# Optimization experiments

Measured on AMD Instinct MI355X. Metric: run time of the kernel, lower is better.

Reference implementation:

```python
import jax, jax.numpy as jnp
import numpy as np

NEG_INF = -1e9


def setup_inputs() -> dict:
    key = jax.random.key(0)
    k1, k2, k3, k4, k5, k6 = jax.random.split(key, 6)
    B, P, N, C, H = 32, 512, 64, 9, 128
    polylines = jax.random.normal(k1, (B, P, N, C), dtype=jnp.float32)
    polylines_mask = jax.random.uniform(k2, (B, P, N)) > 0.1
    # MLP params (Linear(C,H) -> ReLU -> Linear(H,H)), torch-style init scale
    W1 = jax.random.uniform(k3, (C, H), minval=-1.0, maxval=1.0) / jnp.sqrt(C)
    b1 = jax.random.uniform(k4, (H,), minval=-1.0, maxval=1.0) / jnp.sqrt(C)
    W2 = jax.random.uniform(k5, (H, H), minval=-1.0, maxval=1.0) / jnp.sqrt(H)
    b2 = jax.random.uniform(k6, (H,), minval=-1.0, maxval=1.0) / jnp.sqrt(H)
    return {"polylines": polylines, "polylines_mask": polylines_mask,
            "W1": W1, "b1": b1, "W2": W2, "b2": b2}


def reference(polylines, polylines_mask, W1, b1, W2, b2):
    # Point MLP applied to all points (invalid ones are overwritten below,
    # identical math to the torch masked-gather version).
    h = jax.nn.relu(jnp.einsum('bpnc,ch->bpnh', polylines, W1) + b1)
    feat = jnp.einsum('bpnh,hd->bpnd', h, W2) + b2  # [B,P,N,H]
    feat = jnp.where(polylines_mask[..., None], feat, NEG_INF)
    pooled = jnp.max(feat, axis=2)  # [B,P,H]
    # Polylines with no valid points pooled to NEG_INF -> zero them out.
    any_valid = jnp.any(polylines_mask, axis=2)  # [B,P]
    return jnp.where(any_valid[..., None], pooled, 0.0)
```

## Files before the change

### kernel.cpp

```cpp
#include <hip/hip_runtime.h>


using bf16x8 = __attribute__((ext_vector_type(8))) short;
using f32x4  = __attribute__((ext_vector_type(4))) float;

#define MFMA_BF16(A,B,C) __builtin_amdgcn_mfma_f32_16x16x32_bf16((A),(B),(C),0,0,0)

__device__ __forceinline__ unsigned short f2bf(float f) {
  union { float f; unsigned int u; } v; v.f = f;
  unsigned int r = v.u + 0x7fffu + ((v.u >> 16) & 1u);
  return (unsigned short)(r >> 16);
}

__device__ __forceinline__ unsigned int pack_bf2(float a, float b) {
  union { float f; unsigned int u; } ua, ub; ua.f = a; ub.f = b;
  return __builtin_amdgcn_perm(ub.u + 0x8000u, ua.u + 0x8000u, 0x07060302u);
}

__global__ void prep_kernel(const float* __restrict__ W1, const float* __restrict__ W2,
                            const void* __restrict__ mask,
                            unsigned short* __restrict__ w1t, unsigned short* __restrict__ w2t,
                            int* __restrict__ flag) {
  int b = blockIdx.x, t = threadIdx.x;
  if (b < 68) {
    int idx = b * 256 + t;
    if (idx < 128 * 136) {
      int d = idx / 136, h = idx - d * 136;
      float v = (h < 128) ? W2[h * 128 + d] : 0.f;
      w2t[idx] = f2bf(v);
    }
  } else if (b < 88) {
    int idx = (b - 68) * 256 + t;
    if (idx < 128 * 40) {
      int h = idx / 40, c = idx - h * 40;
      float v = (c < 9) ? W1[c * 128 + h] : 0.f;
      w1t[idx] = f2bf(v);
    }
  } else {
    __shared__ int cnt;
    if (t == 0) cnt = 0;
    __syncthreads();
    const unsigned char* mb = (const unsigned char*)mask;
    int local = 0;
    for (int i = t * 16; i < t * 16 + 16; i++) local += (mb[i] != 0) ? 1 : 0;
    atomicAdd(&cnt, local);
    __syncthreads();
    if (t == 0) *flag = (cnt > 2800) ? 1 : 0;
  }
}

__global__ __launch_bounds__(256, 4) void poly_main_k(
    const float* __restrict__ X, const void* __restrict__ mask,
    const float* __restrict__ b1g, const float* __restrict__ b2g,
    const unsigned short* __restrict__ w1t, const unsigned short* __restrict__ w2t,
    const int* __restrict__ flagp, float* __restrict__ out)
{
  __shared__ __align__(16) unsigned short Hb[128 * 136];

  const int tid  = threadIdx.x;
  const int lane = tid & 63;
  const int w    = tid >> 6;
  const int wr   = w >> 1, wc = w & 1;
  const int li   = lane & 15, q = lane >> 4;

  float mf[4];
  {
    int flag = *flagp;
    long long mbase = (long long)blockIdx.x * 128 + wc * 64 + li;
    if (flag) {
      const unsigned char* mp = (const unsigned char*)mask;
      #pragma unroll
      for (int tm = 0; tm < 4; tm++) mf[tm] = mp[mbase + tm * 16] ? 0.f : -4e9f;
    } else {
      const int* mp = (const int*)mask;
      #pragma unroll
      for (int tm = 0; tm < 4; tm++) mf[tm] = mp[mbase + tm * 16] ? 0.f : -4e9f;
    }
  }

  bf16x8 bx[4];
  {
    const float* xb = X + (long long)blockIdx.x * (128 * 9);
    #pragma unroll
    for (int tm = 0; tm < 4; tm++) {
      int m = wc * 64 + tm * 16 + li;
      const float* xr = xb + m * 9;
      union { bf16x8 v; unsigned int u[4]; } uu;
      uu.u[0] = uu.u[1] = uu.u[2] = uu.u[3] = 0u;
      if (q == 0) {
        uu.u[0] = pack_bf2(xr[0], xr[1]);
        uu.u[1] = pack_bf2(xr[2], xr[3]);
        uu.u[2] = pack_bf2(xr[4], xr[5]);
        uu.u[3] = pack_bf2(xr[6], xr[7]);
      } else if (q == 1) {
        uu.u[0] = pack_bf2(xr[8], 0.f);
      }
      bx[tm] = uu.v;
    }
  }

  f32x4 acc1[4][4];
  #pragma unroll
  for (int a = 0; a < 4; a++)
    #pragma unroll
    for (int b = 0; b < 4; b++) acc1[a][b] = f32x4{0.f, 0.f, 0.f, 0.f};
  {
    bf16x8 af[4];
    #pragma unroll
    for (int th = 0; th < 4; th++)
      af[th] = *(const bf16x8*)(w1t + (wr * 64 + th * 16 + li) * 40 + q * 8);
    #pragma unroll
    for (int th = 0; th < 4; th++)
      #pragma unroll
      for (int tm = 0; tm < 4; tm++)
        acc1[th][tm] = MFMA_BF16(af[th], bx[tm], acc1[th][tm]);
  }

  #pragma unroll
  for (int th = 0; th < 4; th++) {
    f32x4 bv = *(const f32x4*)(b1g + wr * 64 + th * 16 + q * 4);
    #pragma unroll
    for (int tm = 0; tm < 4; tm++) {
      int m = wc * 64 + tm * 16 + li;
      float v0 = fmaxf(acc1[th][tm][0] + bv[0], 0.f);
      float v1 = fmaxf(acc1[th][tm][1] + bv[1], 0.f);
      float v2 = fmaxf(acc1[th][tm][2] + bv[2], 0.f);
      float v3 = fmaxf(acc1[th][tm][3] + bv[3], 0.f);
      uint2 hv;
      hv.x = pack_bf2(v0, v1);
      hv.y = pack_bf2(v2, v3);
      *(uint2*)(Hb + m * 136 + wr * 64 + th * 16 + q * 4) = hv;
    }
  }
  __syncthreads();

  f32x4 acc2[4][4];
  #pragma unroll
  for (int a = 0; a < 4; a++)
    #pragma unroll
    for (int b = 0; b < 4; b++) acc2[a][b] = f32x4{0.f, 0.f, 0.f, 0.f};
  #pragma unroll
  for (int ks = 0; ks < 4; ks++) {
    bf16x8 af[4], bf[4];
    #pragma unroll
    for (int td = 0; td < 4; td++)
      af[td] = *(const bf16x8*)(w2t + (wr * 64 + td * 16 + li) * 136 + ks * 32 + q * 8);
    #pragma unroll
    for (int tm = 0; tm < 4; tm++)
      bf[tm] = *(const bf16x8*)(Hb + (wc * 64 + tm * 16 + li) * 136 + ks * 32 + q * 8);
    #pragma unroll
    for (int td = 0; td < 4; td++)
      #pragma unroll
      for (int tm = 0; tm < 4; tm++)
        acc2[td][tm] = MFMA_BF16(af[td], bf[tm], acc2[td][tm]);
  }

  f32x4 pooled[4];
  #pragma unroll
  for (int td = 0; td < 4; td++) {
    f32x4 bv = *(const f32x4*)(b2g + wr * 64 + td * 16 + q * 4);
    #pragma unroll
    for (int r = 0; r < 4; r++) {
      float v0 = acc2[td][0][r] + mf[0];
      float v1 = acc2[td][1][r] + mf[1];
      float v2 = acc2[td][2][r] + mf[2];
      float v3 = acc2[td][3][r] + mf[3];
      pooled[td][r] = fmaxf(fmaxf(v0, v1), fmaxf(v2, v3)) + bv[r];
    }
  }

  #pragma unroll
  for (int s = 8; s >= 1; s >>= 1) {
    #pragma unroll
    for (int td = 0; td < 4; td++) {
      #pragma unroll
      for (int r = 0; r < 4; r++) {
        float o = __shfl_xor(pooled[td][r], s, 64);
        pooled[td][r] = fmaxf(pooled[td][r], o);
      }
    }
  }

  if (li == 0) {
    long long poly = (long long)blockIdx.x * 2 + wc;
    #pragma unroll
    for (int td = 0; td < 4; td++) {
      f32x4 v = pooled[td];
      #pragma unroll
      for (int r = 0; r < 4; r++) if (v[r] < -1e8f) v[r] = 0.f;
      *(f32x4*)(out + poly * 128 + wr * 64 + td * 16 + q * 4) = v;
    }
  }
}

extern "C" void kernel_launch(void* const* d_in, const int* in_sizes, int n_in,
                              void* d_out, int out_size, void* d_ws, size_t ws_size,
                              hipStream_t stream) {
  const float* X    = (const float*)d_in[0];
  const void*  mask = d_in[1];
  const float* W1   = (const float*)d_in[2];
  const float* b1   = (const float*)d_in[3];
  const float* W2   = (const float*)d_in[4];
  const float* b2   = (const float*)d_in[5];
  float* out = (float*)d_out;

  unsigned short* w1t = (unsigned short*)d_ws;
  unsigned short* w2t = w1t + 128 * 40;
  int* flag = (int*)((char*)d_ws + 45056);

  prep_kernel<<<89, 256, 0, stream>>>(W1, W2, mask, w1t, w2t, flag);
  poly_main_k<<<8192, 256, 0, stream>>>(X, mask, b1, b2, w1t, w2t, flag, out);
}
```

Before: 168.1 us.

## Pre-swizzle weights to MFMA fragment order, stage X in LDS, bitpack mask

Weights are now pre-swizzled into per-lane MFMA fragment order, so each lane's global load is contiguous. The X tile is staged through shared memory with coalesced vector loads instead of strided 9-float row reads. A new prep kernel packs the mask into 64-bit ballot bitmasks so the main kernel reads one word per wave. The final pooling reduction moves from cross-lane shuffles to an LDS transpose with coalesced output stores, at the cost of an extra kernel launch and two additional barriers.

```diff
diff --git a/kernel.cpp b/kernel.cpp
--- a/kernel.cpp
+++ b/kernel.cpp
@@ -4,7 +4,7 @@
 using bf16x8 = __attribute__((ext_vector_type(8))) short;
 using f32x4  = __attribute__((ext_vector_type(4))) float;
 
-#define MFMA_BF16(A,B,C) __builtin_amdgcn_mfma_f32_16x16x32_bf16((A),(B),(C),0,0,0)
+#define MFMA32(A,B,C) __builtin_amdgcn_mfma_f32_16x16x32_bf16((A),(B),(C),0,0,0)
 
 __device__ __forceinline__ unsigned short f2bf(float f) {
   union { float f; unsigned int u; } v; v.f = f;
@@ -17,26 +17,12 @@
   return __builtin_amdgcn_perm(ub.u + 0x8000u, ua.u + 0x8000u, 0x07060302u);
 }
 
-__global__ void prep_kernel(const float* __restrict__ W1, const float* __restrict__ W2,
-                            const void* __restrict__ mask,
-                            unsigned short* __restrict__ w1t, unsigned short* __restrict__ w2t,
-                            int* __restrict__ flag) {
+__global__ void prep1(const float* __restrict__ W1, const float* __restrict__ W2,
+                      const void* __restrict__ mask,
+                      unsigned short* __restrict__ w1sw, unsigned short* __restrict__ w2sw,
+                      int* __restrict__ flag) {
   int b = blockIdx.x, t = threadIdx.x;
-  if (b < 68) {
-    int idx = b * 256 + t;
-    if (idx < 128 * 136) {
-      int d = idx / 136, h = idx - d * 136;
-      float v = (h < 128) ? W2[h * 128 + d] : 0.f;
-      w2t[idx] = f2bf(v);
-    }
-  } else if (b < 88) {
-    int idx = (b - 68) * 256 + t;
-    if (idx < 128 * 40) {
-      int h = idx / 40, c = idx - h * 40;
-      float v = (c < 9) ? W1[c * 128 + h] : 0.f;
-      w1t[idx] = f2bf(v);
-    }
-  } else {
+  if (b == 0) {
     __shared__ int cnt;
     if (t == 0) cnt = 0;
     __syncthreads();
@@ -46,15 +32,53 @@
     atomicAdd(&cnt, local);
     __syncthreads();
     if (t == 0) *flag = (cnt > 2800) ? 1 : 0;
-  }
+  } else if (b <= 2) {
+    int e = (b - 1) * 256 + t;
+    int lane = e & 63, grp = e >> 6;
+    int li = lane & 15, q = lane >> 4;
+    int h = grp * 16 + li;
+    int c0 = q * 8;
+    #pragma unroll
+    for (int j = 0; j < 8; j++) {
+      int c = c0 + j;
+      w1sw[e * 8 + j] = f2bf((c < 9) ? W1[c * 128 + h] : 0.f);
+    }
+  } else {
+    int e = (b - 3) * 256 + t;
+    if (e < 2048) {
+      int lane = e & 63, grp = e >> 6;
+      int wr = grp >> 4, sub = grp & 15;
+      int ks = sub >> 2, td = sub & 3;
+      int li = lane & 15, q = lane >> 4;
+      int d = wr * 64 + td * 16 + li;
+      int h0 = ks * 32 + q * 8;
+      #pragma unroll
+      for (int j = 0; j < 8; j++)
+        w2sw[e * 8 + j] = f2bf(W2[(h0 + j) * 128 + d]);
+    }
+  }
+}
+
+__global__ void prep2(const void* __restrict__ mask, const int* __restrict__ flagp,
+                      unsigned long long* __restrict__ bits) {
+  int gid = blockIdx.x * 256 + threadIdx.x;
+  int flag = *flagp;
+  bool v;
+  if (flag) v = ((const unsigned char*)mask)[gid] != 0;
+  else      v = ((const int*)mask)[gid] != 0;
+  unsigned long long bm = __ballot(v);
+  if ((threadIdx.x & 63) == 0)
+    bits[blockIdx.x * 4 + (threadIdx.x >> 6)] = bm;
 }
 
 __global__ __launch_bounds__(256, 4) void poly_main_k(
     const float* __restrict__ X, const void* __restrict__ mask,
     const float* __restrict__ b1g, const float* __restrict__ b2g,
-    const unsigned short* __restrict__ w1t, const unsigned short* __restrict__ w2t,
-    const int* __restrict__ flagp, float* __restrict__ out)
+    const unsigned short* __restrict__ w1sw, const unsigned short* __restrict__ w2sw,
+    const int* __restrict__ flagp, const unsigned long long* __restrict__ bits,
+    int use_bits, float* __restrict__ out)
 {
+  __shared__ __align__(16) float Xs[1152];
   __shared__ __align__(16) unsigned short Hb[128 * 136];
 
   const int tid  = threadIdx.x;
@@ -64,39 +88,47 @@
   const int li   = lane & 15, q = lane >> 4;
 
   float mf[4];
-  {
+  if (use_bits) {
+    unsigned long long bm = bits[(long long)blockIdx.x * 2 + wc];
+    #pragma unroll
+    for (int tm = 0; tm < 4; tm++)
+      mf[tm] = ((bm >> (tm * 16 + li)) & 1ull) ? 0.f : -4e9f;
+  } else {
     int flag = *flagp;
-    long long mbase = (long long)blockIdx.x * 128 + wc * 64 + li;
+    long long mb = (long long)blockIdx.x * 128 + wc * 64 + li;
     if (flag) {
       const unsigned char* mp = (const unsigned char*)mask;
       #pragma unroll
-      for (int tm = 0; tm < 4; tm++) mf[tm] = mp[mbase + tm * 16] ? 0.f : -4e9f;
+      for (int tm = 0; tm < 4; tm++) mf[tm] = mp[mb + tm * 16] ? 0.f : -4e9f;
     } else {
       const int* mp = (const int*)mask;
       #pragma unroll
-      for (int tm = 0; tm < 4; tm++) mf[tm] = mp[mbase + tm * 16] ? 0.f : -4e9f;
-    }
-  }
+      for (int tm = 0; tm < 4; tm++) mf[tm] = mp[mb + tm * 16] ? 0.f : -4e9f;
+    }
+  }
+
+  {
+    const f32x4* xg = (const f32x4*)(X + (long long)blockIdx.x * 1152);
+    f32x4* xl = (f32x4*)Xs;
+    xl[tid] = xg[tid];
+    if (tid < 32) xl[tid + 256] = xg[tid + 256];
+  }
+  __syncthreads();
 
   bf16x8 bx[4];
-  {
-    const float* xb = X + (long long)blockIdx.x * (128 * 9);
-    #pragma unroll
-    for (int tm = 0; tm < 4; tm++) {
-      int m = wc * 64 + tm * 16 + li;
-      const float* xr = xb + m * 9;
-      union { bf16x8 v; unsigned int u[4]; } uu;
-      uu.u[0] = uu.u[1] = uu.u[2] = uu.u[3] = 0u;
-      if (q == 0) {
-        uu.u[0] = pack_bf2(xr[0], xr[1]);
-        uu.u[1] = pack_bf2(xr[2], xr[3]);
-        uu.u[2] = pack_bf2(xr[4], xr[5]);
-        uu.u[3] = pack_bf2(xr[6], xr[7]);
-      } else if (q == 1) {
-        uu.u[0] = pack_bf2(xr[8], 0.f);
-      }
-      bx[tm] = uu.v;
-    }
+  #pragma unroll
+  for (int tm = 0; tm < 4; tm++) {
+    int m = wc * 64 + tm * 16 + li;
+    const float* xr = Xs + m * 9;
+    union { bf16x8 v; unsigned int u[4]; } uu;
+    uu.u[0] = uu.u[1] = uu.u[2] = uu.u[3] = 0u;
+    if (q == 0) {
+      uu.u[0] = pack_bf2(xr[0], xr[1]); uu.u[1] = pack_bf2(xr[2], xr[3]);
+      uu.u[2] = pack_bf2(xr[4], xr[5]); uu.u[3] = pack_bf2(xr[6], xr[7]);
+    } else if (q == 1) {
+      uu.u[0] = pack_bf2(xr[8], 0.f);
+    }
+    bx[tm] = uu.v;
   }
 
   f32x4 acc1[4][4];
@@ -105,15 +137,15 @@
     #pragma unroll
     for (int b = 0; b < 4; b++) acc1[a][b] = f32x4{0.f, 0.f, 0.f, 0.f};
   {
-    bf16x8 af[4];
+    bf16x8 a1[4];
     #pragma unroll
     for (int th = 0; th < 4; th++)
-      af[th] = *(const bf16x8*)(w1t + (wr * 64 + th * 16 + li) * 40 + q * 8);
+      a1[th] = *(const bf16x8*)(w1sw + ((wr * 4 + th) * 64 + lane) * 8);
     #pragma unroll
     for (int th = 0; th < 4; th++)
       #pragma unroll
       for (int tm = 0; tm < 4; tm++)
-        acc1[th][tm] = MFMA_BF16(af[th], bx[tm], acc1[th][tm]);
+        acc1[th][tm] = MFMA32(a1[th], bx[tm], acc1[th][tm]);
   }
 
   #pragma unroll
@@ -141,18 +173,18 @@
     for (int b = 0; b < 4; b++) acc2[a][b] = f32x4{0.f, 0.f, 0.f, 0.f};
   #pragma unroll
   for (int ks = 0; ks < 4; ks++) {
-    bf16x8 af[4], bf[4];
+    bf16x8 a2[4], bb[4];
     #pragma unroll
     for (int td = 0; td < 4; td++)
-      af[td] = *(const bf16x8*)(w2t + (wr * 64 + td * 16 + li) * 136 + ks * 32 + q * 8);
+      a2[td] = *(const bf16x8*)(w2sw + (((wr * 16 + ks * 4 + td) * 64) + lane) * 8);
     #pragma unroll
     for (int tm = 0; tm < 4; tm++)
-      bf[tm] = *(const bf16x8*)(Hb + (wc * 64 + tm * 16 + li) * 136 + ks * 32 + q * 8);
+      bb[tm] = *(const bf16x8*)(Hb + (wc * 64 + tm * 16 + li) * 136 + ks * 32 + q * 8);
     #pragma unroll
     for (int td = 0; td < 4; td++)
       #pragma unroll
       for (int tm = 0; tm < 4; tm++)
-        acc2[td][tm] = MFMA_BF16(af[td], bf[tm], acc2[td][tm]);
+        acc2[td][tm] = MFMA32(a2[td], bb[tm], acc2[td][tm]);
   }
 
   f32x4 pooled[4];
@@ -169,27 +201,21 @@
     }
   }
 
-  #pragma unroll
-  for (int s = 8; s >= 1; s >>= 1) {
-    #pragma unroll
-    for (int td = 0; td < 4; td++) {
-      #pragma unroll
-      for (int r = 0; r < 4; r++) {
-        float o = __shfl_xor(pooled[td][r], s, 64);
-        pooled[td][r] = fmaxf(pooled[td][r], o);
-      }
-    }
-  }
-
-  if (li == 0) {
-    long long poly = (long long)blockIdx.x * 2 + wc;
-    #pragma unroll
-    for (int td = 0; td < 4; td++) {
-      f32x4 v = pooled[td];
-      #pragma unroll
-      for (int r = 0; r < 4; r++) if (v[r] < -1e8f) v[r] = 0.f;
-      *(f32x4*)(out + poly * 128 + wr * 64 + td * 16 + q * 4) = v;
-    }
+  __syncthreads();
+  float* P = (float*)Hb;
+  #pragma unroll
+  for (int td = 0; td < 4; td++)
+    *(f32x4*)(P + (wc * 16 + li) * 132 + wr * 64 + td * 16 + q * 4) = pooled[td];
+  __syncthreads();
+
+  {
+    int p = tid >> 7, d = tid & 127;
+    const float* Pp = P + p * (16 * 132) + d;
+    float v = Pp[0];
+    #pragma unroll
+    for (int j = 1; j < 16; j++) v = fmaxf(v, Pp[j * 132]);
+    if (v < -1e8f) v = 0.f;
+    out[(long long)blockIdx.x * 256 + tid] = v;
   }
 }
 
@@ -204,10 +230,14 @@
   const float* b2   = (const float*)d_in[5];
   float* out = (float*)d_out;
 
-  unsigned short* w1t = (unsigned short*)d_ws;
-  unsigned short* w2t = w1t + 128 * 40;
-  int* flag = (int*)((char*)d_ws + 45056);
-
-  prep_kernel<<<89, 256, 0, stream>>>(W1, W2, mask, w1t, w2t, flag);
-  poly_main_k<<<8192, 256, 0, stream>>>(X, mask, b1, b2, w1t, w2t, flag, out);
-}
+  unsigned short* w1sw = (unsigned short*)d_ws;
+  unsigned short* w2sw = (unsigned short*)((char*)d_ws + 8192);
+  int* flag            = (int*)((char*)d_ws + 40960);
+  unsigned long long* bits = (unsigned long long*)((char*)d_ws + 49152);
+  int use_bits = (ws_size >= (size_t)(49152 + 131072)) ? 1 : 0;
+
+  prep1<<<11, 256, 0, stream>>>(W1, W2, mask, w1sw, w2sw, flag);
+  if (use_bits) prep2<<<4096, 256, 0, stream>>>(mask, flag, bits);
+  poly_main_k<<<8192, 256, 0, stream>>>(X, mask, b1, b2, w1sw, w2sw, flag, bits,
+                                        use_bits, out);
+}
```

Result: faster. 143.1 us (-14.9%).
